# Optimization experiments

Measured on AMD Instinct MI355X. Metric: run time of the kernel, lower is better.

The kernel has to match this reference:

```python
import math
import jax, jax.numpy as jnp
import numpy as np

B, QL, CL, D, H = 4, 2048, 2048, 512, 8  # batch, q_len, c_len, hidden/query/context dim, heads
A = D // H
SCALE = 1.0 / math.sqrt(D)
FILL = -100000.0


def setup_inputs() -> dict:
    key = jax.random.key(0)
    ks = jax.random.split(key, 6)
    query = jax.random.normal(ks[0], (B, QL, D), dtype=jnp.float32)
    context = jax.random.normal(ks[1], (B, CL, D), dtype=jnp.float32)
    mask = jax.random.randint(ks[2], (B, CL, H), 0, 2).astype(bool)
    Wq = (jax.random.normal(ks[3], (D, D)) * 0.02).astype(jnp.float32)    # Q: query_dim -> hidden_dim (no bias)
    Wkv = (jax.random.normal(ks[4], (D, 2 * D)) * 0.02).astype(jnp.float32)  # KV: context_dim -> 2*hidden_dim
    Wout = (jax.random.normal(ks[5], (D, D)) * 0.02).astype(jnp.float32)  # out: hidden_dim -> context_dim
    return {"query": query, "context": context, "mask": mask, "Wq": Wq, "Wkv": Wkv, "Wout": Wout}


def reference(query, context, mask, Wq, Wkv, Wout):
    b, q_len, _ = query.shape
    c_len = context.shape[1]
    q = (query @ Wq).reshape(b, q_len, H, A)
    kv = context @ Wkv
    k = kv[..., :D].reshape(b, c_len, H, A)
    v = kv[..., D:].reshape(b, c_len, H, A)
    # [b, q, k, h] scores
    scores = jnp.einsum('bqha,bkha->bqkh', q, k)
    # mask.unsqueeze(1): [b, 1, c_len, h]; apply_mask == where(mask, FILL, x)
    scores = jnp.where(mask[:, None, :, :], FILL, scores)
    attn_weights = jax.nn.softmax(scores * SCALE, axis=2)
    # NOTE: faithful to original torch einsum 'bqkh,bvha->bqha' (k and v are
    # independent summed indices, as in the source code).
    attn = jnp.einsum('bqkh,bvha->bqha', attn_weights, v)
    attn = attn.reshape(b, q_len, D)
    return attn @ Wout
```

## Files before the change

### kernel.cpp

```cpp
#include <hip/hip_runtime.h>

#define BATCH 4
#define QLEN 2048
#define CLEN 2048
#define DIM 512
#define NCH 64
#define NBLK1 (BATCH * NCH)
#define NSL 8


__global__ __launch_bounds__(256) void k1_partial(const float* __restrict__ ctx,
                                                  float4* __restrict__ partial) {
    __shared__ float4 red[256];
    const int blk = blockIdx.x, t = threadIdx.x;
    const int b = blk >> 6, ch = blk & 63;
    const int rg = t >> 7, f4 = t & 127;
    const float4* src = reinterpret_cast<const float4*>(ctx)
                      + (size_t)(b * CLEN + ch * 32 + rg) * (DIM / 4) + f4;
    float4 s0 = make_float4(0.f, 0.f, 0.f, 0.f);
    float4 s1 = make_float4(0.f, 0.f, 0.f, 0.f);
#pragma unroll
    for (int i = 0; i < 16; i += 2) {
        float4 x = src[(size_t)(2 * i) * (DIM / 4)];
        float4 y = src[(size_t)(2 * i + 2) * (DIM / 4)];
        s0.x += x.x; s0.y += x.y; s0.z += x.z; s0.w += x.w;
        s1.x += y.x; s1.y += y.y; s1.z += y.z; s1.w += y.w;
    }
    red[t] = make_float4(s0.x + s1.x, s0.y + s1.y, s0.z + s1.z, s0.w + s1.w);
    __syncthreads();
    if (t < 128) {
        float4 a = red[t], c = red[t + 128];
        partial[(size_t)blk * (DIM / 4) + t] =
            make_float4(a.x + c.x, a.y + c.y, a.z + c.z, a.w + c.w);
    }
}

__global__ __launch_bounds__(256) void k2_middle(const float4* __restrict__ partial4,
                                                 const float* __restrict__ Wkv,
                                                 const float* __restrict__ Wout,
                                                 float* __restrict__ opart) {
    __shared__ float4 csh[2][128];
    __shared__ float cs[DIM];
    __shared__ float vl[256];
    __shared__ float vslice[64];
    const int blk = blockIdx.x, t = threadIdx.x;
    const int b = blk >> 3, sl = blk & 7;

    {
        const int f4 = t & 127, h = t >> 7;
        const float4* p = partial4 + (size_t)(b * NCH + h * 32) * (DIM / 4) + f4;
        float4 s = make_float4(0.f, 0.f, 0.f, 0.f);
#pragma unroll 8
        for (int ch = 0; ch < 32; ++ch) {
            float4 x = p[(size_t)ch * (DIM / 4)];
            s.x += x.x; s.y += x.y; s.z += x.z; s.w += x.w;
        }
        csh[h][f4] = s;
    }
    __syncthreads();
    if (t < 128) {
        float4 a = csh[0][t], c = csh[1][t];
        reinterpret_cast<float4*>(cs)[t] =
            make_float4(a.x + c.x, a.y + c.y, a.z + c.z, a.w + c.w);
    }
    __syncthreads();

    {
        const int el = t & 63, dg = t >> 6;
        const float* w = Wkv + (size_t)(dg * 128) * (2 * DIM) + DIM + sl * 64 + el;
        float s = 0.f;
#pragma unroll 8
        for (int d0 = 0; d0 < 128; ++d0)
            s += cs[dg * 128 + d0] * w[(size_t)d0 * (2 * DIM)];
        vl[t] = s;
    }
    __syncthreads();
    if (t < 64) vslice[t] = vl[t] + vl[t + 64] + vl[t + 128] + vl[t + 192];
    __syncthreads();

#pragma unroll
    for (int half = 0; half < 2; ++half) {
        const int f = half * 256 + t;
        const float* w = Wout + (size_t)(sl * 64) * DIM + f;
        float s = 0.f;
#pragma unroll 8
        for (int e0 = 0; e0 < 64; ++e0) s += vslice[e0] * w[(size_t)e0 * DIM];
        opart[(size_t)(sl * BATCH + b) * DIM + f] = s;
    }
}

__global__ __launch_bounds__(256) void k3_bcast(const float4* __restrict__ opart4,
                                                float4* __restrict__ out) {
    const int blk = blockIdx.x, t = threadIdx.x;
    const int b = blk >> 8, qg = blk & 255;
    const int rg = t >> 7, f4 = t & 127;
    float4 v = make_float4(0.f, 0.f, 0.f, 0.f);
#pragma unroll
    for (int sl = 0; sl < NSL; ++sl) {
        float4 x = opart4[(size_t)(sl * BATCH + b) * (DIM / 4) + f4];
        v.x += x.x; v.y += x.y; v.z += x.z; v.w += x.w;
    }
    float4* dst = out + (size_t)(b * QLEN + qg * 8) * (DIM / 4);
#pragma unroll
    for (int i = 0; i < 4; ++i)
        dst[(size_t)(rg + 2 * i) * (DIM / 4) + f4] = v;
}

extern "C" void kernel_launch(void* const* d_in, const int* in_sizes, int n_in,
                              void* d_out, int out_size, void* d_ws, size_t ws_size,
                              hipStream_t stream) {
    const float* ctx  = (const float*)d_in[1];
    const float* Wkv  = (const float*)d_in[4];
    const float* Wout = (const float*)d_in[5];
    float* ws = (float*)d_ws;
    float* partial = ws;
    float* opart   = partial + (size_t)NBLK1 * DIM;

    k1_partial<<<NBLK1, 256, 0, stream>>>(ctx, (float4*)partial);
    k2_middle<<<BATCH * NSL, 256, 0, stream>>>((const float4*)partial, Wkv, Wout, opart);
    k3_bcast<<<BATCH * 256, 256, 0, stream>>>((const float4*)opart, (float4*)d_out);
}
```

Baseline: 28.98 us.

## Fuse three kernels into one persistent kernel with atomic-counter grid synchronization

Replaces the three-launch pipeline (context column-sum, V/Wout projection, broadcast) with a single 256-block kernel. The last eight blocks to finish per batch do the projection slices, and all blocks spin on per-batch atomic counters before broadcasting the result rows. Partial sums and outputs go through relaxed agent-scope atomic loads and stores. This removes two kernel launches and their gaps, at the cost of a memset, spin-waits that assume all 256 blocks are co-resident, and relaxed ordering that could be fragile.

Result: slower. 37.24 us (+28.5%).

```diff
diff --git a/kernel.cpp b/kernel.cpp
--- a/kernel.cpp
+++ b/kernel.cpp
@@ -4,106 +4,139 @@
 #define QLEN 2048
 #define CLEN 2048
 #define DIM 512
-#define NCH 64
-#define NBLK1 (BATCH * NCH)
-#define NSL 8
+#define NBLK 256
+#define BPB 64
+#define ROWS 32
+#define NFIN 8
 
 
-__global__ __launch_bounds__(256) void k1_partial(const float* __restrict__ ctx,
-                                                  float4* __restrict__ partial) {
+typedef unsigned long long u64;
+
+__device__ __forceinline__ float2 u2f(u64 v) {
+    union { u64 u; float2 f; } c; c.u = v; return c.f;
+}
+__device__ __forceinline__ u64 f2u(float x, float y) {
+    union { u64 u; float2 f; } c; c.f = make_float2(x, y); return c.u;
+}
+__device__ __forceinline__ u64 ald(const u64* p) {
+    return __hip_atomic_load(p, __ATOMIC_RELAXED, __HIP_MEMORY_SCOPE_AGENT);
+}
+__device__ __forceinline__ void ast(u64* p, u64 v) {
+    __hip_atomic_store(p, v, __ATOMIC_RELAXED, __HIP_MEMORY_SCOPE_AGENT);
+}
+
+__global__ __launch_bounds__(256, 2) void k_fused(
+    const float* __restrict__ ctx, const float* __restrict__ Wkv,
+    const float* __restrict__ Wout, u64* __restrict__ partial_u,
+    float* __restrict__ opart, unsigned* __restrict__ ctrA,
+    unsigned* __restrict__ ctrB, float4* __restrict__ out)
+{
     __shared__ float4 red[256];
+    __shared__ float cs[DIM];
+    __shared__ float vl[256];
+    __shared__ float vsl[64];
+    __shared__ float orow[DIM];
+    __shared__ unsigned s_old;
     const int blk = blockIdx.x, t = threadIdx.x;
     const int b = blk >> 6, ch = blk & 63;
     const int rg = t >> 7, f4 = t & 127;
-    const float4* src = reinterpret_cast<const float4*>(ctx)
-                      + (size_t)(b * CLEN + ch * 32 + rg) * (DIM / 4) + f4;
-    float4 s0 = make_float4(0.f, 0.f, 0.f, 0.f);
-    float4 s1 = make_float4(0.f, 0.f, 0.f, 0.f);
-#pragma unroll
-    for (int i = 0; i < 16; i += 2) {
-        float4 x = src[(size_t)(2 * i) * (DIM / 4)];
-        float4 y = src[(size_t)(2 * i + 2) * (DIM / 4)];
-        s0.x += x.x; s0.y += x.y; s0.z += x.z; s0.w += x.w;
-        s1.x += y.x; s1.y += y.y; s1.z += y.z; s1.w += y.w;
-    }
-    red[t] = make_float4(s0.x + s1.x, s0.y + s1.y, s0.z + s1.z, s0.w + s1.w);
-    __syncthreads();
-    if (t < 128) {
-        float4 a = red[t], c = red[t + 128];
-        partial[(size_t)blk * (DIM / 4) + t] =
-            make_float4(a.x + c.x, a.y + c.y, a.z + c.z, a.w + c.w);
-    }
-}
-
-__global__ __launch_bounds__(256) void k2_middle(const float4* __restrict__ partial4,
-                                                 const float* __restrict__ Wkv,
-                                                 const float* __restrict__ Wout,
-                                                 float* __restrict__ opart) {
-    __shared__ float4 csh[2][128];
-    __shared__ float cs[DIM];
-    __shared__ float vl[256];
-    __shared__ float vslice[64];
-    const int blk = blockIdx.x, t = threadIdx.x;
-    const int b = blk >> 3, sl = blk & 7;
 
     {
-        const int f4 = t & 127, h = t >> 7;
-        const float4* p = partial4 + (size_t)(b * NCH + h * 32) * (DIM / 4) + f4;
-        float4 s = make_float4(0.f, 0.f, 0.f, 0.f);
+        const float4* src = reinterpret_cast<const float4*>(ctx)
+                          + (size_t)(b * CLEN + ch * ROWS + rg) * (DIM / 4) + f4;
+        float4 s0 = make_float4(0.f, 0.f, 0.f, 0.f);
+        float4 s1 = make_float4(0.f, 0.f, 0.f, 0.f);
+#pragma unroll
+        for (int i = 0; i < 16; i += 2) {
+            float4 x = src[(size_t)(2 * i) * (DIM / 4)];
+            float4 y = src[(size_t)(2 * i + 2) * (DIM / 4)];
+            s0.x += x.x; s0.y += x.y; s0.z += x.z; s0.w += x.w;
+            s1.x += y.x; s1.y += y.y; s1.z += y.z; s1.w += y.w;
+        }
+        red[t] = make_float4(s0.x + s1.x, s0.y + s1.y, s0.z + s1.z, s0.w + s1.w);
+        __syncthreads();
+        if (t < 128) {
+            float4 a = red[t], c = red[t + 128];
+            u64* dst = partial_u + (size_t)(b * BPB + ch) * 256 + 2 * t;
+            ast(dst,     f2u(a.x + c.x, a.y + c.y));
+            ast(dst + 1, f2u(a.z + c.z, a.w + c.w));
+        }
+        __syncthreads();
+        if (t == 0)
+            s_old = __hip_atomic_fetch_add(&ctrA[b], 1u, __ATOMIC_RELAXED,
+                                           __HIP_MEMORY_SCOPE_AGENT);
+        __syncthreads();
+    }
+
+    if (s_old >= BPB - NFIN) {
+        const int sl = (int)s_old - (BPB - NFIN);
+        if (t == 0)
+            while (__hip_atomic_load(&ctrA[b], __ATOMIC_RELAXED,
+                                     __HIP_MEMORY_SCOPE_AGENT) < BPB)
+                __builtin_amdgcn_s_sleep(2);
+        __syncthreads();
+        {
+            const u64* pb = partial_u + (size_t)(b * BPB) * 256 + t;
+            float ax = 0.f, ay = 0.f;
 #pragma unroll 8
-        for (int ch = 0; ch < 32; ++ch) {
-            float4 x = p[(size_t)ch * (DIM / 4)];
-            s.x += x.x; s.y += x.y; s.z += x.z; s.w += x.w;
+            for (int c = 0; c < BPB; ++c) {
+                float2 v = u2f(ald(pb + (size_t)c * 256));
+                ax += v.x; ay += v.y;
+            }
+            cs[2 * t] = ax; cs[2 * t + 1] = ay;
         }
-        csh[h][f4] = s;
+        __syncthreads();
+        {
+            const int el = t & 63, dg = t >> 6;
+            const float* w = Wkv + (size_t)(dg * 128) * (2 * DIM) + DIM + sl * 64 + el;
+            float s = 0.f;
+#pragma unroll 8
+            for (int d0 = 0; d0 < 128; ++d0)
+                s += cs[dg * 128 + d0] * w[(size_t)d0 * (2 * DIM)];
+            vl[t] = s;
+        }
+        __syncthreads();
+        if (t < 64) vsl[t] = vl[t] + vl[t + 64] + vl[t + 128] + vl[t + 192];
+        __syncthreads();
+#pragma unroll
+        for (int half = 0; half < 2; ++half) {
+            const int f = half * 256 + t;
+            const float* w = Wout + (size_t)(sl * 64) * DIM + f;
+            float s = 0.f;
+#pragma unroll 8
+            for (int e0 = 0; e0 < 64; ++e0) s += vsl[e0] * w[(size_t)e0 * DIM];
+            __hip_atomic_store(&opart[(size_t)(sl * BATCH + b) * DIM + f], s,
+                               __ATOMIC_RELAXED, __HIP_MEMORY_SCOPE_AGENT);
+        }
+        __syncthreads();
+        if (t == 0)
+            __hip_atomic_fetch_add(&ctrB[b], 1u, __ATOMIC_RELAXED,
+                                   __HIP_MEMORY_SCOPE_AGENT);
+    }
+
+    if (t == 0)
+        while (__hip_atomic_load(&ctrB[b], __ATOMIC_RELAXED,
+                                 __HIP_MEMORY_SCOPE_AGENT) < NFIN)
+            __builtin_amdgcn_s_sleep(4);
+    __syncthreads();
+    {
+        const u64* ob = reinterpret_cast<const u64*>(opart) + b * 256 + t;
+        float ax = 0.f, ay = 0.f;
+#pragma unroll
+        for (int sl = 0; sl < NFIN; ++sl) {
+            float2 v = u2f(ald(ob + (size_t)sl * BATCH * 256));
+            ax += v.x; ay += v.y;
+        }
+        orow[2 * t] = ax; orow[2 * t + 1] = ay;
     }
     __syncthreads();
-    if (t < 128) {
-        float4 a = csh[0][t], c = csh[1][t];
-        reinterpret_cast<float4*>(cs)[t] =
-            make_float4(a.x + c.x, a.y + c.y, a.z + c.z, a.w + c.w);
+    {
+        const float4 val = reinterpret_cast<const float4*>(orow)[f4];
+        float4* dst = out + (size_t)(b * QLEN + ch * ROWS + rg) * (DIM / 4) + f4;
+#pragma unroll
+        for (int i = 0; i < 16; ++i)
+            dst[(size_t)(2 * i) * (DIM / 4)] = val;
     }
-    __syncthreads();
-
-    {
-        const int el = t & 63, dg = t >> 6;
-        const float* w = Wkv + (size_t)(dg * 128) * (2 * DIM) + DIM + sl * 64 + el;
-        float s = 0.f;
-#pragma unroll 8
-        for (int d0 = 0; d0 < 128; ++d0)
-            s += cs[dg * 128 + d0] * w[(size_t)d0 * (2 * DIM)];
-        vl[t] = s;
-    }
-    __syncthreads();
-    if (t < 64) vslice[t] = vl[t] + vl[t + 64] + vl[t + 128] + vl[t + 192];
-    __syncthreads();
-
-#pragma unroll
-    for (int half = 0; half < 2; ++half) {
-        const int f = half * 256 + t;
-        const float* w = Wout + (size_t)(sl * 64) * DIM + f;
-        float s = 0.f;
-#pragma unroll 8
-        for (int e0 = 0; e0 < 64; ++e0) s += vslice[e0] * w[(size_t)e0 * DIM];
-        opart[(size_t)(sl * BATCH + b) * DIM + f] = s;
-    }
-}
-
-__global__ __launch_bounds__(256) void k3_bcast(const float4* __restrict__ opart4,
-                                                float4* __restrict__ out) {
-    const int blk = blockIdx.x, t = threadIdx.x;
-    const int b = blk >> 8, qg = blk & 255;
-    const int rg = t >> 7, f4 = t & 127;
-    float4 v = make_float4(0.f, 0.f, 0.f, 0.f);
-#pragma unroll
-    for (int sl = 0; sl < NSL; ++sl) {
-        float4 x = opart4[(size_t)(sl * BATCH + b) * (DIM / 4) + f4];
-        v.x += x.x; v.y += x.y; v.z += x.z; v.w += x.w;
-    }
-    float4* dst = out + (size_t)(b * QLEN + qg * 8) * (DIM / 4);
-#pragma unroll
-    for (int i = 0; i < 4; ++i)
-        dst[(size_t)(rg + 2 * i) * (DIM / 4) + f4] = v;
 }
 
 extern "C" void kernel_launch(void* const* d_in, const int* in_sizes, int n_in,
@@ -112,11 +145,12 @@
     const float* ctx  = (const float*)d_in[1];
     const float* Wkv  = (const float*)d_in[4];
     const float* Wout = (const float*)d_in[5];
-    float* ws = (float*)d_ws;
-    float* partial = ws;
-    float* opart   = partial + (size_t)NBLK1 * DIM;
+    unsigned* ctrA = (unsigned*)d_ws;
+    unsigned* ctrB = ctrA + 4;
+    u64* partial_u = (u64*)((char*)d_ws + 64);
+    float* opart   = (float*)((char*)d_ws + 64 + 524288);
 
-    k1_partial<<<NBLK1, 256, 0, stream>>>(ctx, (float4*)partial);
-    k2_middle<<<BATCH * NSL, 256, 0, stream>>>((const float4*)partial, Wkv, Wout, opart);
-    k3_bcast<<<BATCH * 256, 256, 0, stream>>>((const float4*)opart, (float4*)d_out);
+    hipMemsetAsync(d_ws, 0, 64, stream);
+    k_fused<<<NBLK, 256, 0, stream>>>(ctx, Wkv, Wout, partial_u, opart,
+                                      ctrA, ctrB, (float4*)d_out);
 }
```

## Split context-sum reduction into wider partials plus dedicated reduce kernel

Applied to the files above, without the earlier changes.

The column-sum over context rows now uses 1024 partial rows of 8 context rows each, written by 512 blocks with nontemporal loads and no shared-memory reduction. A new reduce kernel spreads the final 256-way reduction per batch across 512 blocks, instead of having each of the 32 middle blocks serially re-read 64 partial rows. The broadcast kernel now writes 16 rows per block with nontemporal stores. The cost is an extra kernel launch and a larger partial buffer written to and read back from memory.

New measurement: 26.26 us. -9.4%, faster.

```diff
diff --git a/kernel.cpp b/kernel.cpp
--- a/kernel.cpp
+++ b/kernel.cpp
@@ -4,67 +4,55 @@
 #define QLEN 2048
 #define CLEN 2048
 #define DIM 512
-#define NCH 64
-#define NBLK1 (BATCH * NCH)
+#define CPB 256
 #define NSL 8
 
 
+typedef float f32x4 __attribute__((ext_vector_type(4)));
+
 __global__ __launch_bounds__(256) void k1_partial(const float* __restrict__ ctx,
-                                                  float4* __restrict__ partial) {
-    __shared__ float4 red[256];
-    const int blk = blockIdx.x, t = threadIdx.x;
-    const int b = blk >> 6, ch = blk & 63;
-    const int rg = t >> 7, f4 = t & 127;
-    const float4* src = reinterpret_cast<const float4*>(ctx)
-                      + (size_t)(b * CLEN + ch * 32 + rg) * (DIM / 4) + f4;
-    float4 s0 = make_float4(0.f, 0.f, 0.f, 0.f);
-    float4 s1 = make_float4(0.f, 0.f, 0.f, 0.f);
+                                                  f32x4* __restrict__ partial) {
+    const int t = threadIdx.x;
+    const int c = blockIdx.x * 2 + (t >> 7);
+    const int f4 = t & 127;
+    const f32x4* src = reinterpret_cast<const f32x4*>(ctx)
+                     + (size_t)c * 8 * (DIM / 4) + f4;
+    f32x4 s0 = {0.f, 0.f, 0.f, 0.f}, s1 = {0.f, 0.f, 0.f, 0.f};
 #pragma unroll
-    for (int i = 0; i < 16; i += 2) {
-        float4 x = src[(size_t)(2 * i) * (DIM / 4)];
-        float4 y = src[(size_t)(2 * i + 2) * (DIM / 4)];
-        s0.x += x.x; s0.y += x.y; s0.z += x.z; s0.w += x.w;
-        s1.x += y.x; s1.y += y.y; s1.z += y.z; s1.w += y.w;
+    for (int r = 0; r < 8; r += 2) {
+        s0 += __builtin_nontemporal_load(&src[(size_t)r * (DIM / 4)]);
+        s1 += __builtin_nontemporal_load(&src[(size_t)(r + 1) * (DIM / 4)]);
     }
-    red[t] = make_float4(s0.x + s1.x, s0.y + s1.y, s0.z + s1.z, s0.w + s1.w);
-    __syncthreads();
-    if (t < 128) {
-        float4 a = red[t], c = red[t + 128];
-        partial[(size_t)blk * (DIM / 4) + t] =
-            make_float4(a.x + c.x, a.y + c.y, a.z + c.z, a.w + c.w);
-    }
+    partial[(size_t)c * (DIM / 4) + f4] = s0 + s1;
 }
 
-__global__ __launch_bounds__(256) void k2_middle(const float4* __restrict__ partial4,
-                                                 const float* __restrict__ Wkv,
-                                                 const float* __restrict__ Wout,
-                                                 float* __restrict__ opart) {
-    __shared__ float4 csh[2][128];
+__global__ __launch_bounds__(256) void k2_reduce(const f32x4* __restrict__ partial,
+                                                 f32x4* __restrict__ csum) {
+    __shared__ f32x4 red[256];
+    const int blk = blockIdx.x, t = threadIdx.x;
+    const int b = blk >> 7, f4g = blk & 127;
+    red[t] = partial[(size_t)(b * CPB + t) * (DIM / 4) + f4g];
+    __syncthreads();
+#pragma unroll
+    for (int s = 128; s > 0; s >>= 1) {
+        if (t < s) red[t] += red[t + s];
+        __syncthreads();
+    }
+    if (t == 0) csum[b * (DIM / 4) + f4g] = red[0];
+}
+
+__global__ __launch_bounds__(256) void k3_mid(const float* __restrict__ csum,
+                                              const float* __restrict__ Wkv,
+                                              const float* __restrict__ Wout,
+                                              float* __restrict__ opart) {
     __shared__ float cs[DIM];
     __shared__ float vl[256];
     __shared__ float vslice[64];
     const int blk = blockIdx.x, t = threadIdx.x;
     const int b = blk >> 3, sl = blk & 7;
-
-    {
-        const int f4 = t & 127, h = t >> 7;
-        const float4* p = partial4 + (size_t)(b * NCH + h * 32) * (DIM / 4) + f4;
-        float4 s = make_float4(0.f, 0.f, 0.f, 0.f);
-#pragma unroll 8
-        for (int ch = 0; ch < 32; ++ch) {
-            float4 x = p[(size_t)ch * (DIM / 4)];
-            s.x += x.x; s.y += x.y; s.z += x.z; s.w += x.w;
-        }
-        csh[h][f4] = s;
-    }
+    cs[t] = csum[b * DIM + t];
+    cs[t + 256] = csum[b * DIM + t + 256];
     __syncthreads();
-    if (t < 128) {
-        float4 a = csh[0][t], c = csh[1][t];
-        reinterpret_cast<float4*>(cs)[t] =
-            make_float4(a.x + c.x, a.y + c.y, a.z + c.z, a.w + c.w);
-    }
-    __syncthreads();
-
     {
         const int el = t & 63, dg = t >> 6;
         const float* w = Wkv + (size_t)(dg * 128) * (2 * DIM) + DIM + sl * 64 + el;
@@ -77,7 +65,6 @@
     __syncthreads();
     if (t < 64) vslice[t] = vl[t] + vl[t + 64] + vl[t + 128] + vl[t + 192];
     __syncthreads();
-
 #pragma unroll
     for (int half = 0; half < 2; ++half) {
         const int f = half * 256 + t;
@@ -89,21 +76,19 @@
     }
 }
 
-__global__ __launch_bounds__(256) void k3_bcast(const float4* __restrict__ opart4,
-                                                float4* __restrict__ out) {
+__global__ __launch_bounds__(256) void k4_bcast(const f32x4* __restrict__ opart4,
+                                                f32x4* __restrict__ out) {
     const int blk = blockIdx.x, t = threadIdx.x;
-    const int b = blk >> 8, qg = blk & 255;
+    const int b = blk >> 7, qg = blk & 127;
     const int rg = t >> 7, f4 = t & 127;
-    float4 v = make_float4(0.f, 0.f, 0.f, 0.f);
+    f32x4 v = {0.f, 0.f, 0.f, 0.f};
 #pragma unroll
-    for (int sl = 0; sl < NSL; ++sl) {
-        float4 x = opart4[(size_t)(sl * BATCH + b) * (DIM / 4) + f4];
-        v.x += x.x; v.y += x.y; v.z += x.z; v.w += x.w;
-    }
-    float4* dst = out + (size_t)(b * QLEN + qg * 8) * (DIM / 4);
+    for (int sl = 0; sl < NSL; ++sl)
+        v += opart4[(size_t)(sl * BATCH + b) * (DIM / 4) + f4];
+    f32x4* dst = out + (size_t)(b * QLEN + qg * 16) * (DIM / 4) + f4;
 #pragma unroll
-    for (int i = 0; i < 4; ++i)
-        dst[(size_t)(rg + 2 * i) * (DIM / 4) + f4] = v;
+    for (int i = 0; i < 8; ++i)
+        __builtin_nontemporal_store(v, &dst[(size_t)(rg + 2 * i) * (DIM / 4)]);
 }
 
 extern "C" void kernel_launch(void* const* d_in, const int* in_sizes, int n_in,
@@ -114,9 +99,11 @@
     const float* Wout = (const float*)d_in[5];
     float* ws = (float*)d_ws;
     float* partial = ws;
-    float* opart   = partial + (size_t)NBLK1 * DIM;
+    float* csum    = partial + (size_t)1024 * DIM;
+    float* opart   = csum + BATCH * DIM;
 
-    k1_partial<<<NBLK1, 256, 0, stream>>>(ctx, (float4*)partial);
-    k2_middle<<<BATCH * NSL, 256, 0, stream>>>((const float4*)partial, Wkv, Wout, opart);
-    k3_bcast<<<BATCH * 256, 256, 0, stream>>>((const float4*)opart, (float4*)d_out);
+    k1_partial<<<512, 256, 0, stream>>>(ctx, (f32x4*)partial);
+    k2_reduce<<<512, 256, 0, stream>>>((const f32x4*)partial, (f32x4*)csum);
+    k3_mid<<<BATCH * NSL, 256, 0, stream>>>(csum, Wkv, Wout, opart);
+    k4_bcast<<<512, 256, 0, stream>>>((const f32x4*)opart, (f32x4*)d_out);
 }
```
